# Kernel tuning notes

Measured on AMD Instinct MI355X. Metric: run time of the kernel, lower is better.

## Reference

```python
import jax, jax.numpy as jnp
import numpy as np

B, T, H, W, C = 2, 8, 20, 36, 512
NH = 4
HD = C // NH
WS = (5, 9)
EXP = (2, 4)              # window_size // 2
KP = (5, 9)               # focal unfold kernel for level k=0
PADP = (2, 4)
T2T_K, T2T_S, T2T_P = (7, 7), (3, 3), (3, 3)
FFN_HD = 1960
NWH, NWW = H // WS[0], W // WS[1]   # 4, 4
WAREA = WS[0] * WS[1]               # 45


def _valid_ind_rolled():
    wh, ww = WS
    eh, ew = EXP
    m = np.ones((4, wh, ww), np.float32)
    m[0, :wh - eh, :ww - ew] = 0   # tl
    m[1, :wh - eh, ew:] = 0        # tr
    m[2, eh:, :ww - ew] = 0        # bl
    m[3, eh:, ew:] = 0             # br
    return jnp.asarray(np.nonzero(m.reshape(-1))[0])

VALID_ROLLED = _valid_ind_rolled()  # (120,)


def unfold(x, k, s, p):
    # x: (N, Cc, Hh, Ww) -> (N, Cc*kh*kw, L); matches torch.nn.Unfold layout (c slowest).
    N, Cc, Hh, Ww = x.shape
    kh, kw = k; sh, sw = s; ph, pw = p
    xp = jnp.pad(x, ((0, 0), (0, 0), (ph, ph), (pw, pw)))
    oh = (Hh + 2 * ph - kh) // sh + 1
    ow = (Ww + 2 * pw - kw) // sw + 1
    cols = [xp[:, :, i:i + oh * sh:sh, j:j + ow * sw:sw]
            for i in range(kh) for j in range(kw)]
    patches = jnp.stack(cols, axis=2)            # (N, Cc, kh*kw, oh, ow)
    return patches.reshape(N, Cc * kh * kw, oh * ow)


def fold(patches, out_hw, k, s, p):
    # inverse of unfold (overlap-add), matches torch F.fold.
    N = patches.shape[0]
    kh, kw = k; sh, sw = s; ph, pw = p
    Hh, Ww = out_hw
    oh = (Hh + 2 * ph - kh) // sh + 1
    ow = (Ww + 2 * pw - kw) // sw + 1
    Cc = patches.shape[1] // (kh * kw)
    pr = patches.reshape(N, Cc, kh, kw, oh, ow)
    out = jnp.zeros((N, Cc, Hh + 2 * ph, Ww + 2 * pw), patches.dtype)
    for i in range(kh):
        for j in range(kw):
            out = out.at[:, :, i:i + oh * sh:sh, j:j + ow * sw:sw].add(pr[:, :, i, j])
    return out[:, :, ph:ph + Hh, pw:pw + Ww]


def layer_norm(x, g, b):
    mu = jnp.mean(x, -1, keepdims=True)
    var = jnp.var(x, -1, keepdims=True)
    return (x - mu) * jax.lax.rsqrt(var + 1e-5) * g + b


def win_part(x):
    # (B,T,H,W,C) -> (B*nW, T*wh*ww, C)
    b = x.shape[0]
    x = x.reshape(b, T, NWH, WS[0], NWW, WS[1], C)
    return x.transpose(0, 2, 4, 1, 3, 5, 6).reshape(-1, T * WAREA, C)


def to_heads(w):
    return w.reshape(-1, T, WAREA, NH, HD).transpose(0, 3, 1, 2, 4).reshape(-1, NH, T * WAREA, HD)


def block_forward(x, g1, be1, wqkv, bqkv, wproj, bproj, wpool, bpool, g2, be2, w1, bf1, w2, bf2, out_h, out_w):
    shortcut = x
    xn = layer_norm(x, g1, be1)

    # ---- coarser (pooled) focal level, k=0 (focal_level=2) ----
    wnr = xn.reshape(B, T, NWH, WS[0], NWW, WS[1], C).transpose(0, 2, 4, 1, 3, 5, 6)
    wnr = wnr.reshape(B, NWH, NWW, T, WAREA, C)
    pooled = jnp.einsum('bhwtnc,n->bhwtc', wnr, wpool) + bpool   # (B,NWH,NWW,T,C)

    # ---- window attention ----
    qkv = xn @ wqkv + bqkv                                       # (B,T,H,W,3C)
    q, k, v = jnp.split(qkv, 3, axis=-1)
    qw = to_heads(win_part(q)) * (HD ** -0.5)
    kw_, vw = to_heads(win_part(k)), to_heads(win_part(v))

    def rolled(t):
        parts = []
        for sh, sw in ((-EXP[0], -EXP[1]), (-EXP[0], EXP[1]), (EXP[0], -EXP[1]), (EXP[0], EXP[1])):
            r = jnp.roll(t, (sh, sw), axis=(2, 3))
            parts.append(win_part(r).reshape(-1, T, WAREA, NH, HD))
        cat = jnp.concatenate(parts, axis=2)                     # (B*nW, T, 4*warea, NH, HD)
        cat = jnp.take(cat.transpose(0, 3, 1, 2, 4), VALID_ROLLED, axis=3)
        return cat.reshape(-1, NH, T * VALID_ROLLED.shape[0], HD)

    k_rolled = jnp.concatenate([kw_, rolled(k)], axis=2)         # (B*nW, NH, T*165, HD)
    v_rolled = jnp.concatenate([vw, rolled(v)], axis=2)

    # pooled keys/values via focal unfold
    xp = pooled.transpose(0, 3, 1, 2, 4)                          # (B,T,NWH,NWW,C)
    qkv_p = xp @ wqkv + bqkv
    kp, vp = qkv_p[..., C:2 * C], qkv_p[..., 2 * C:]

    def unfold_kv(t):
        t = t.transpose(0, 1, 4, 2, 3).reshape(B * T, C, NWH, NWW)
        u = unfold(t, KP, (1, 1), PADP)                           # (B*T, C*45, L)
        L = u.shape[-1]
        u = u.reshape(B, T, C, KP[0], KP[1], L).transpose(0, 5, 1, 3, 4, 2)
        u = u.reshape(B * L, T, KP[0] * KP[1], NH, HD).transpose(0, 3, 1, 2, 4)
        return u.reshape(B * L, NH, T * KP[0] * KP[1], HD)

    k_all = jnp.concatenate([k_rolled, unfold_kv(kp)], axis=2)
    v_all = jnp.concatenate([v_rolled, unfold_kv(vp)], axis=2)

    attn = jnp.einsum('wnqd,wnkd->wnqk', qw, k_all)               # (B*nW, NH, T*45, N)

    # validity mask for pooled context (zero-padded unfold positions -> -100)
    ones = jnp.ones((T, 1, NWH, NWW), x.dtype)
    um = unfold(ones, KP, (1, 1), PADP)                           # (T, 45, L)
    L = um.shape[-1]
    mvals = jnp.where(um.reshape(T, KP[0] * KP[1], L).transpose(2, 0, 1).reshape(L, -1) == 0,
                      jnp.asarray(-100.0, x.dtype), jnp.asarray(0.0, x.dtype))
    n_rolled = k_rolled.shape[2]
    mask_cols = jnp.concatenate([jnp.zeros((L, n_rolled), x.dtype), mvals], axis=1)
    attn = attn + jnp.tile(mask_cols, (B, 1))[:, None, None, :]

    attn = jax.nn.softmax(attn, axis=-1)
    out = jnp.einsum('wnqk,wnkd->wnqd', attn, v_all)
    out = out.transpose(0, 2, 1, 3).reshape(-1, T * WAREA, C) @ wproj + bproj

    # window reverse + residual
    out = out.reshape(B, NWH, NWW, T, WS[0], WS[1], C)
    out = out.transpose(0, 3, 1, 4, 2, 5, 6).reshape(B, T, H, W, C)
    x = shortcut + out

    # ---- FusionFeedForward (fold/unfold re-normalized MLP) ----
    y = layer_norm(x, g2, be2).reshape(B, T * H * W, C)
    h = y @ w1 + bf1                                              # (B, n, 1960)
    nvec = ((out_h + 2 * T2T_P[0] - T2T_K[0]) // T2T_S[0] + 1) * \
           ((out_w + 2 * T2T_P[1] - T2T_K[1]) // T2T_S[1] + 1)
    bt = (B * T * H * W) // nvec
    norm_p = jnp.ones((bt, T2T_K[0] * T2T_K[1], nvec), x.dtype)
    norm_f = fold(norm_p, (out_h, out_w), T2T_K, T2T_S, T2T_P)    # (bt,1,out_h,out_w)
    h_f = fold(h.reshape(bt, nvec, FFN_HD).transpose(0, 2, 1), (out_h, out_w), T2T_K, T2T_S, T2T_P)
    h = unfold(h_f / norm_f, T2T_K, T2T_S, T2T_P).transpose(0, 2, 1).reshape(B, T * H * W, FFN_HD)
    h = jax.nn.gelu(h, approximate=False) @ w2 + bf2
    return x + h.reshape(B, T, H, W, C)


def setup_inputs() -> dict:
    key = jax.random.key(0)
    ks = jax.random.split(key, 8)
    s = 0.02
    return dict(
        x=jax.random.normal(ks[0], (B, T, H, W, C), jnp.float32),
        g1=jnp.ones((C,), jnp.float32),
        be1=jnp.zeros((C,), jnp.float32),
        wqkv=jax.random.normal(ks[1], (C, 3 * C), jnp.float32) * s,
        bqkv=jnp.zeros((3 * C,), jnp.float32),
        wproj=jax.random.normal(ks[2], (C, C), jnp.float32) * s,
        bproj=jnp.zeros((C,), jnp.float32),
        wpool=jnp.full((WAREA,), 1.0 / WAREA, jnp.float32),
        bpool=jnp.zeros((1,), jnp.float32),
        g2=jnp.ones((C,), jnp.float32),
        be2=jnp.zeros((C,), jnp.float32),
        w1=jax.random.normal(ks[3], (C, FFN_HD), jnp.float32) * s,
        bf1=jnp.zeros((FFN_HD,), jnp.float32),
        w2=jax.random.normal(ks[4], (FFN_HD, C), jnp.float32) * s,
        bf2=jnp.zeros((C,), jnp.float32),
        out_h=60,
        out_w=108,
    )


def reference(x, g1, be1, wqkv, bqkv, wproj, bproj, wpool, bpool, g2, be2, w1, bf1, w2, bf2, out_h, out_w):
    return block_forward(x, g1, be1, wqkv, bqkv, wproj, bproj, wpool, bpool,
                         g2, be2, w1, bf1, w2, bf2, out_h, out_w)
```

## Files before the change

### kernel.cpp

```cpp
#include <hip/hip_runtime.h>
#include <hip/hip_bf16.h>
#include <math.h>

typedef __hip_bfloat16 bf16;
typedef __attribute__((ext_vector_type(8))) short bf16x8;
typedef __attribute__((ext_vector_type(4))) float f32x4;

#define DEVI __device__ __forceinline__

#define C_ 512
#define NH_ 4
#define NTOK 11520
#define NKEY 1680
#define NRK 120
#define FFN_ 1960
#define ZROW (NTOK + 256)

DEVI float ldf(const bf16* p) { return __bfloat162float(*p); }
DEVI float ldf(const float* p) { return *p; }
DEVI void stw(bf16* p, float v) { *p = __float2bfloat16(v); }
DEVI void stw(float* p, float v) { *p = v; }
DEVI unsigned short f2bs(float f) { bf16 h = __float2bfloat16(f); return *(unsigned short*)&h; }

template <int DT> DEVI float ldw(const void* p, size_t i) {
  if (DT == 0) return __bfloat162float(((const bf16*)p)[i]);
  else         return ((const float*)p)[i];
}

DEVI void gload_lds16(const void* g, void* l) {
  __builtin_amdgcn_global_load_lds(
      (const __attribute__((address_space(1))) void*)g,
      (__attribute__((address_space(3))) void*)l, 16, 0, 0);
}

__global__ void k_detect(const void* __restrict__ g1, int* __restrict__ flag) {
  if (threadIdx.x == 0) {
    const unsigned short* p = (const unsigned short*)g1;
    *flag = (p[0] == 0x3F80u) ? 0 : 1;
  }
}

__global__ void k_prep(int* __restrict__ table) {
  if (threadIdx.x == 0) {
    int cnt = 0;
    for (int p = 0; p < 4; p++)
      for (int wi = 0; wi < 5; wi++)
        for (int wj = 0; wj < 9; wj++) {
          bool invalid;
          if (p == 0)      invalid = (wi < 3) && (wj < 5);
          else if (p == 1) invalid = (wi < 3) && (wj >= 4);
          else if (p == 2) invalid = (wi >= 2) && (wj < 5);
          else             invalid = (wi >= 2) && (wj >= 4);
          if (!invalid) table[cnt++] = p * 45 + wi * 9 + wj;
        }
  }
}

__global__ void k_ksrc(const int* __restrict__ vtab, int* __restrict__ ksrc) {
  int idx = blockIdx.x * 256 + threadIdx.x;
  if (idx >= 32 * NKEY) return;
  int w = idx / NKEY, j = idx % NKEY;
  int b = w >> 4, nh = (w >> 2) & 3, nw = w & 3;
  int val;
  if (j < 360) {
    int t = j / 45, pos = j % 45, wi = pos / 9, wj2 = pos % 9;
    val = ((b * 8 + t) * 20 + nh * 5 + wi) * 36 + nw * 9 + wj2;
  } else if (j < 1320) {
    int jj = j - 360;
    int t = jj / 120, r = jj % 120;
    int id = vtab[r];
    int p = id / 45, pos = id % 45, wi = pos / 9, wj2 = pos % 9;
    int sh = (p < 2) ? -2 : 2;
    int sw = (p & 1) ? 4 : -4;
    int hh = nh * 5 + wi - sh;
    if (hh < 0) hh += 20; else if (hh >= 20) hh -= 20;
    int ww2 = nw * 9 + wj2 - sw;
    if (ww2 < 0) ww2 += 36; else if (ww2 >= 36) ww2 -= 36;
    val = ((b * 8 + t) * 20 + hh) * 36 + ww2;
  } else {
    int jj = j - 1320;
    int t = jj / 45, kidx = jj % 45, ki = kidx / 9, kj = kidx % 9;
    int snh = nh + ki - 2, snw = nw + kj - 4;
    if (snh < 0 || snh >= 4 || snw < 0 || snw >= 4) val = -1;
    else val = NTOK + (b * 8 + t) * 16 + snh * 4 + snw;
  }
  ksrc[idx] = val;
}

template <int DT>
__global__ void k_wcvt(const int* __restrict__ dflag, const void* __restrict__ in,
                       bf16* __restrict__ out, int K, int N, int Npad) {
  if (*dflag != DT) return;
  __shared__ float t[64][65];
  const int n0 = blockIdx.x * 64;
  const int k0 = blockIdx.y * 64;
  const int tx = threadIdx.x & 63, tg = threadIdx.x >> 6;
#pragma unroll
  for (int r = 0; r < 16; r++) {
    int k = k0 + r * 4 + tg;
    int nn = n0 + tx;
    float v = (k < K && nn < N) ? ldw<DT>(in, (size_t)k * N + nn) : 0.f;
    t[r * 4 + tg][tx] = v;
  }
  __syncthreads();
#pragma unroll
  for (int r = 0; r < 16; r++) {
    int nn = n0 + r * 4 + tg;
    int k = k0 + tx;
    if (nn < Npad && k < K)
      out[(size_t)nn * K + k] = __float2bfloat16(t[tx][r * 4 + tg]);
  }
}

template <int DT>
__global__ void k_bcvt(const int* __restrict__ dflag, const void* __restrict__ in,
                       float* __restrict__ out, int n) {
  if (*dflag != DT) return;
  int i = blockIdx.x * 256 + threadIdx.x;
  if (i < n) out[i] = ldw<DT>(in, i);
}

__global__ void k_zrow(bf16* __restrict__ p) {
  p[blockIdx.x * 256 + threadIdx.x] = __float2bfloat16(0.f);
}

template <int DT, typename InT>
__global__ void k_ln(const int* __restrict__ dflag, const InT* __restrict__ xin,
                     const void* __restrict__ g, const void* __restrict__ be,
                     bf16* __restrict__ out) {
  if (*dflag != DT) return;
  const int tok = blockIdx.x;
  const int tid = threadIdx.x;
  const size_t base = (size_t)tok * C_;
  float v0 = ldf(xin + base + tid);
  float v1 = ldf(xin + base + tid + 256);
  float s = v0 + v1, ss = v0 * v0 + v1 * v1;
#pragma unroll
  for (int o = 32; o; o >>= 1) { s += __shfl_xor(s, o); ss += __shfl_xor(ss, o); }
  __shared__ float sh[10];
  const int lane = tid & 63, wv = tid >> 6;
  if (lane == 0) { sh[wv] = s; sh[4 + wv] = ss; }
  __syncthreads();
  if (tid == 0) {
    float a = sh[0] + sh[1] + sh[2] + sh[3];
    float q = sh[4] + sh[5] + sh[6] + sh[7];
    float mu = a * (1.0f / C_);
    float var = q * (1.0f / C_) - mu * mu;
    sh[8] = mu; sh[9] = rsqrtf(fmaxf(var, 0.f) + 1e-5f);
  }
  __syncthreads();
  float mu = sh[8], inv = sh[9];
  stw(out + base + tid,
      (v0 - mu) * inv * ldw<DT>(g, tid) + ldw<DT>(be, tid));
  stw(out + base + tid + 256,
      (v1 - mu) * inv * ldw<DT>(g, tid + 256) + ldw<DT>(be, tid + 256));
}

template <int DT>
__global__ void k_pool(const int* __restrict__ dflag, const bf16* __restrict__ xn,
                       const void* __restrict__ wpool, const void* __restrict__ bpool,
                       float* __restrict__ pooled) {
  if (*dflag != DT) return;
  int idx = blockIdx.x * blockDim.x + threadIdx.x;
  if (idx >= 256 * C_) return;
  int c = idx & (C_ - 1);
  int fw = idx >> 9;
  int nw = fw & 3, nh = (fw >> 2) & 3;
  int bt = fw >> 4;
  float acc = ldw<DT>(bpool, 0);
  for (int wi = 0; wi < 5; wi++) {
    int hh = nh * 5 + wi;
    const bf16* base = xn + (((size_t)(bt * 20 + hh)) * 36 + nw * 9) * C_ + c;
    for (int wj = 0; wj < 9; wj++)
      acc += __bfloat162float(base[(size_t)wj * C_]) * ldw<DT>(wpool, wi * 9 + wj);
  }
  pooled[idx] = acc;
}

template <int DT>
__global__ void k_gemm_small(const int* __restrict__ dflag, const float* __restrict__ A,
                             const void* __restrict__ Bw, const void* __restrict__ bias,
                             bf16* __restrict__ Cc) {
  if (*dflag != DT) return;
  __shared__ float As[8][512];
  const int n = blockIdx.x * 256 + threadIdx.x;
  const int m0 = blockIdx.y * 8;
  for (int i = threadIdx.x; i < 8 * 512; i += 256)
    As[i >> 9][i & 511] = A[(size_t)(m0 + (i >> 9)) * 512 + (i & 511)];
  __syncthreads();
  float acc[8];
  float bv = ldw<DT>(bias, n);
#pragma unroll
  for (int mm = 0; mm < 8; mm++) acc[mm] = bv;
  for (int k = 0; k < 512; k++) {
    float b = ldw<DT>(Bw, (size_t)k * 1536 + n);
#pragma unroll
    for (int mm = 0; mm < 8; mm++) acc[mm] += As[mm][k] * b;
  }
#pragma unroll
  for (int mm = 0; mm < 8; mm++)
    Cc[(size_t)(m0 + mm) * 1536 + n] = __float2bfloat16(acc[mm]);
}

template <int DT, int RES, typename OutT>
__global__ __launch_bounds__(256) void k_gemm_m(const int* __restrict__ dflag,
                                                const bf16* __restrict__ A,
                                                const bf16* __restrict__ Bt,
                                                const float* __restrict__ bias,
                                                const void* __restrict__ resid,
                                                OutT* __restrict__ out,
                                                int M, int N, int K) {
  if (dflag && *dflag != DT) return;
  __shared__ __align__(16) unsigned short As[128 * 32];
  __shared__ __align__(16) unsigned short Bs[128 * 32];
  const int tid = threadIdx.x;
  const int lane = tid & 63, wid = tid >> 6;
  const int r15 = lane & 15, quad = lane >> 4;
  const int wm = wid >> 1, wn = wid & 1;
  const int m0 = blockIdx.y * 128, n0 = blockIdx.x * 128;

  f32x4 acc[4][4];
#pragma unroll
  for (int i = 0; i < 4; i++)
#pragma unroll
    for (int j = 0; j < 4; j++)
#pragma unroll
      for (int e = 0; e < 4; e++) acc[i][j][e] = 0.f;

  const int lrow = lane >> 2, lcol = (lane & 3) * 8;

  for (int k0 = 0; k0 < K; k0 += 32) {
    int rem = K - k0;
    if (rem >= 32) {
      const bf16* ga = A + (size_t)(m0 + wid * 32 + lrow) * K + k0 + lcol;
      gload_lds16(ga, &As[wid * 1024]);
      gload_lds16(ga + (size_t)16 * K, &As[wid * 1024 + 512]);
      const bf16* gb = Bt + (size_t)(n0 + wid * 32 + lrow) * K + k0 + lcol;
      gload_lds16(gb, &Bs[wid * 1024]);
      gload_lds16(gb + (size_t)16 * K, &Bs[wid * 1024 + 512]);
    } else {
      int r = tid >> 2, c = (tid & 3) * 8;
      uint4 z = make_uint4(0, 0, 0, 0);
      uint4 a0 = z, a1 = z, b0 = z, b1 = z;
      if (c < rem) {
        a0 = *(const uint4*)(A + (size_t)(m0 + r) * K + k0 + c);
        a1 = *(const uint4*)(A + (size_t)(m0 + r + 64) * K + k0 + c);
        b0 = *(const uint4*)(Bt + (size_t)(n0 + r) * K + k0 + c);
        b1 = *(const uint4*)(Bt + (size_t)(n0 + r + 64) * K + k0 + c);
      }
      *(uint4*)&As[r * 32 + c] = a0;
      *(uint4*)&As[(r + 64) * 32 + c] = a1;
      *(uint4*)&Bs[r * 32 + c] = b0;
      *(uint4*)&Bs[(r + 64) * 32 + c] = b1;
    }
    __syncthreads();

    bf16x8 af[4], bfr[4];
#pragma unroll
    for (int mf = 0; mf < 4; mf++)
      af[mf] = *(const bf16x8*)&As[(wm * 64 + mf * 16 + r15) * 32 + quad * 8];
#pragma unroll
    for (int nf = 0; nf < 4; nf++)
      bfr[nf] = *(const bf16x8*)&Bs[(wn * 64 + nf * 16 + r15) * 32 + quad * 8];
#pragma unroll
    for (int mf = 0; mf < 4; mf++)
#pragma unroll
      for (int nf = 0; nf < 4; nf++)
        acc[mf][nf] = __builtin_amdgcn_mfma_f32_16x16x32_bf16(af[mf], bfr[nf],
                                                              acc[mf][nf], 0, 0, 0);
    __syncthreads();
  }

#pragma unroll
  for (int nf = 0; nf < 4; nf++) {
    int n = n0 + wn * 64 + nf * 16 + r15;
    if (n >= N) continue;
    float bv = bias[n];
#pragma unroll
    for (int mf = 0; mf < 4; mf++) {
      int mb = m0 + wm * 64 + mf * 16 + quad * 4;
#pragma unroll
      for (int e = 0; e < 4; e++) {
        size_t off = (size_t)(mb + e) * N + n;
        float v = acc[mf][nf][e] + bv;
        if (RES == 1) v += ldw<DT>(resid, off);
        else if (RES == 2) v += ((const float*)resid)[off];
        stw(out + off, v);
      }
    }
  }
}

#define KT 64
#define KPAD 136
#define VPAD 72
__global__ __launch_bounds__(768) void k_attn_m(const bf16* __restrict__ qkv,
                                                const int* __restrict__ ksrc,
                                                bf16* __restrict__ ao) {
  __shared__ int ks_l[NKEY];
  __shared__ __align__(16) unsigned short ktl[2][KT * KPAD];
  __shared__ __align__(16) unsigned short vtl[2][128 * VPAD];
  __shared__ __align__(16) unsigned short ptl[12 * 16 * VPAD];
  __shared__ float maskv[2][KT];

  const int tid = threadIdx.x;
  const int lane = tid & 63, wid = tid >> 6;
  const int r15 = lane & 15, quad = lane >> 4;
  const int w = blockIdx.x, qt = blockIdx.y, n = blockIdx.z;
  const int b = w >> 4, nh = (w >> 2) & 3, nw = w & 3;
  const unsigned short* qkvs = (const unsigned short*)qkv;

  for (int j = tid; j < NKEY; j += 768) ks_l[j] = ksrc[w * NKEY + j];

  bf16x8 qf[4];
  {
    int qw = qt * 192 + wid * 16 + r15;
    int qc2 = qw < 360 ? qw : 359;
    int t = qc2 / 45, pos = qc2 % 45, wi = pos / 9, wj = pos % 9;
    int tok = ((b * 8 + t) * 20 + nh * 5 + wi) * 36 + nw * 9 + wj;
    const unsigned short* qp = qkvs + (size_t)tok * 1536 + n * 128 + quad * 8;
#pragma unroll
    for (int c = 0; c < 4; c++)
      qf[c] = *(const bf16x8*)(qp + c * 32);
  }

  f32x4 of[8];
#pragma unroll
  for (int nt = 0; nt < 8; nt++)
#pragma unroll
    for (int e = 0; e < 4; e++) of[nt][e] = 0.f;
  float m_[4], l_[4];
#pragma unroll
  for (int e = 0; e < 4; e++) { m_[e] = -1e30f; l_[e] = 0.f; }

  unsigned short* ptw = &ptl[wid * 16 * VPAD];

  const bool isK = (wid < 4);
  const int kr = tid >> 2, kp = tid & 3;
  const int vr = lane, vp8 = wid - 4;
  uint4 k0, k1, k2, k3, v0, v1;
  float mreg = -30000.f;
  const unsigned short* kbase = qkvs + 512 + n * 128 + kp * 32;
  const unsigned short* vbase = qkvs + 1024 + n * 128 + vp8 * 16;

  auto load_tile = [&](int j0) {
    int cnt = NKEY - j0; if (cnt > KT) cnt = KT;
    if (isK) {
      int s0 = (kr < cnt) ? ks_l[j0 + kr] : -1;
      mreg = (s0 < 0) ? -30000.f : 0.f;
      int row = (s0 < 0) ? ZROW : s0;
      const uint4* kq = (const uint4*)(kbase + (size_t)row * 1536);
      k0 = kq[0]; k1 = kq[1]; k2 = kq[2]; k3 = kq[3];
    } else {
      int s1 = (vr < cnt) ? ks_l[j0 + vr] : -1;
      int row = (s1 < 0) ? ZROW : s1;
      const uint4* vq = (const uint4*)(vbase + (size_t)row * 1536);
      v0 = vq[0]; v1 = vq[1];
    }
  };

  auto store_tile = [&](int buf) {
    if (isK) {
      if (kp == 0) maskv[buf][kr] = mreg;
      unsigned short* kb = &ktl[buf][kr * KPAD + kp * 32];
      *(uint4*)&kb[0]  = k0;
      *(uint4*)&kb[8]  = k1;
      *(uint4*)&kb[16] = k2;
      *(uint4*)&kb[24] = k3;
    } else {
      unsigned short* vb = &vtl[buf][0];
      int d0 = vp8 * 16;
      vb[(d0 + 0) * VPAD + vr]  = (unsigned short)(v0.x & 0xFFFFu);
      vb[(d0 + 1) * VPAD + vr]  = (unsigned short)(v0.x >> 16);
      vb[(d0 + 2) * VPAD + vr]  = (unsigned short)(v0.y & 0xFFFFu);
      vb[(d0 + 3) * VPAD + vr]  = (unsigned short)(v0.y >> 16);
      vb[(d0 + 4) * VPAD + vr]  = (unsigned short)(v0.z & 0xFFFFu);
      vb[(d0 + 5) * VPAD + vr]  = (unsigned short)(v0.z >> 16);
      vb[(d0 + 6) * VPAD + vr]  = (unsigned short)(v0.w & 0xFFFFu);
      vb[(d0 + 7) * VPAD + vr]  = (unsigned short)(v0.w >> 16);
      vb[(d0 + 8) * VPAD + vr]  = (unsigned short)(v1.x & 0xFFFFu);
      vb[(d0 + 9) * VPAD + vr]  = (unsigned short)(v1.x >> 16);
      vb[(d0 + 10) * VPAD + vr] = (unsigned short)(v1.y & 0xFFFFu);
      vb[(d0 + 11) * VPAD + vr] = (unsigned short)(v1.y >> 16);
      vb[(d0 + 12) * VPAD + vr] = (unsigned short)(v1.z & 0xFFFFu);
      vb[(d0 + 13) * VPAD + vr] = (unsigned short)(v1.z >> 16);
      vb[(d0 + 14) * VPAD + vr] = (unsigned short)(v1.w & 0xFFFFu);
      vb[(d0 + 15) * VPAD + vr] = (unsigned short)(v1.w >> 16);
    }
  };

  __syncthreads();
  load_tile(0);
  store_tile(0);
  load_tile(KT);
  __syncthreads();

  int cur = 0, j0 = 0;
  while (true) {
    int nxt = j0 + KT;
    if (nxt < NKEY) {
      store_tile(cur ^ 1);
      if (nxt + KT < NKEY) load_tile(nxt + KT);
    }

    const unsigned short* ktc = &ktl[cur][0];
    const unsigned short* vtc = &vtl[cur][0];
    const float* mkc = maskv[cur];

    f32x4 sf[4];
#pragma unroll
    for (int ft = 0; ft < 4; ft++)
#pragma unroll
      for (int e = 0; e < 4; e++) sf[ft][e] = 0.f;
#pragma unroll
    for (int kc = 0; kc < 4; kc++) {
      bf16x8 a = qf[kc];
#pragma unroll
      for (int ft = 0; ft < 4; ft++) {
        bf16x8 bb = *(const bf16x8*)&ktc[(ft * 16 + r15) * KPAD + kc * 32 + quad * 8];
        sf[ft] = __builtin_amdgcn_mfma_f32_16x16x32_bf16(a, bb, sf[ft], 0, 0, 0);
      }
    }
    const float scl = 0.088388347648318447f;
#pragma unroll
    for (int ft = 0; ft < 4; ft++) {
      float mk = mkc[ft * 16 + r15];
#pragma unroll
      for (int e = 0; e < 4; e++) sf[ft][e] = sf[ft][e] * scl + mk;
    }
    float tm[4];
#pragma unroll
    for (int e = 0; e < 4; e++) {
      float v = fmaxf(fmaxf(sf[0][e], sf[1][e]), fmaxf(sf[2][e], sf[3][e]));
#pragma unroll
      for (int o = 1; o < 16; o <<= 1) v = fmaxf(v, __shfl_xor(v, o));
      tm[e] = v;
    }
#pragma unroll
    for (int e = 0; e < 4; e++) {
      float mn = fmaxf(m_[e], tm[e]);
      float alpha = __expf(m_[e] - mn);
      m_[e] = mn;
      float rs = 0.f;
#pragma unroll
      for (int ft = 0; ft < 4; ft++) {
        float pv = __expf(sf[ft][e] - mn);
        rs += pv;
        ptw[(quad * 4 + e) * VPAD + ft * 16 + r15] = f2bs(pv);
      }
      l_[e] = l_[e] * alpha + rs;
#pragma unroll
      for (int nt = 0; nt < 8; nt++) of[nt][e] *= alpha;
    }
#pragma unroll
    for (int kc = 0; kc < 2; kc++) {
      bf16x8 pa = *(const bf16x8*)&ptw[r15 * VPAD + kc * 32 + quad * 8];
#pragma unroll
      for (int nt = 0; nt < 8; nt++) {
        bf16x8 vb = *(const bf16x8*)&vtc[(nt * 16 + r15) * VPAD + kc * 32 + quad * 8];
        of[nt] = __builtin_amdgcn_mfma_f32_16x16x32_bf16(pa, vb, of[nt], 0, 0, 0);
      }
    }

    if (nxt >= NKEY) break;
    __syncthreads();
    cur ^= 1; j0 = nxt;
  }

#pragma unroll
  for (int e = 0; e < 4; e++) {
#pragma unroll
    for (int o = 1; o < 16; o <<= 1) l_[e] += __shfl_xor(l_[e], o);
  }
#pragma unroll
  for (int e = 0; e < 4; e++) {
    int qw = qt * 192 + wid * 16 + quad * 4 + e;
    if (qw >= 360) continue;
    float inv = 1.0f / l_[e];
    int t = qw / 45, pos = qw % 45, wi = pos / 9, wj = pos % 9;
    int tok = ((b * 8 + t) * 20 + nh * 5 + wi) * 36 + nw * 9 + wj;
    bf16* op = ao + (size_t)tok * 512 + n * 128 + r15;
#pragma unroll
    for (int nt = 0; nt < 8; nt++)
      stw(op + nt * 16, of[nt][e] * inv);
  }
}

__global__ void k_fold(const bf16* __restrict__ h1, float* __restrict__ hf) {
  int idx = blockIdx.x * 256 + threadIdx.x;
  if (idx >= 16 * 40 * 60 * 108) return;
  int x = idx % 108;
  int tmp = idx / 108;
  int y = tmp % 60; tmp /= 60;
  int c = tmp % 40;
  int bt = tmp / 40;
  float sum = 0.f;
  int cnt = 0;
  for (int ki = y % 3; ki < 7; ki += 3) {
    int num = y + 3 - ki;
    if (num < 0) continue;
    int oh = num / 3;
    if (oh >= 20) continue;
    for (int kj = x % 3; kj < 7; kj += 3) {
      int num2 = x + 3 - kj;
      if (num2 < 0) continue;
      int ow = num2 / 3;
      if (ow >= 36) continue;
      sum += __bfloat162float(
          h1[(size_t)(bt * 720 + oh * 36 + ow) * FFN_ + c * 49 + ki * 7 + kj]);
      cnt++;
    }
  }
  hf[idx] = sum / (float)cnt;
}

__global__ void k_unfold_gelu(const float* __restrict__ hf, bf16* __restrict__ h2) {
  int idx = blockIdx.x * 256 + threadIdx.x;
  if (idx >= NTOK * FFN_) return;
  int f = idx % FFN_;
  int token = idx / FFN_;
  int c = f / 49, k = f % 49, ki = k / 7, kj = k % 7;
  int bt = token / 720, vec = token % 720;
  int oh = vec / 36, ow = vec % 36;
  int y = oh * 3 + ki - 3, x = ow * 3 + kj - 3;
  float v = 0.f;
  if (y >= 0 && y < 60 && x >= 0 && x < 108)
    v = hf[((size_t)(bt * 40 + c) * 60 + y) * 108 + x];
  float g = 0.5f * v * (1.0f + erff(v * 0.70710678118654752f));
  stw(h2 + idx, g);
}

extern "C" void kernel_launch(void* const* d_in, const int* in_sizes, int n_in,
                              void* d_out, int out_size, void* d_ws, size_t ws_size,
                              hipStream_t stream) {
  (void)in_sizes; (void)n_in; (void)out_size; (void)ws_size;
  const void* x     = d_in[0];
  const void* g1    = d_in[1];
  const void* be1   = d_in[2];
  const void* wqkv  = d_in[3];
  const void* bqkv  = d_in[4];
  const void* wproj = d_in[5];
  const void* bproj = d_in[6];
  const void* wpool = d_in[7];
  const void* bpool = d_in[8];
  const void* g2    = d_in[9];
  const void* be2   = d_in[10];
  const void* w1    = d_in[11];
  const void* bf1   = d_in[12];
  const void* w2    = d_in[13];
  const void* bf2   = d_in[14];

  char* ws = (char*)d_ws;
  size_t off = 0;
  auto alloc = [&](size_t bytes) -> void* {
    void* p = ws + off;
    off += (bytes + 255) & ~(size_t)255;
    return p;
  };

  int*   dflag  = (int*)  alloc(256);
  int*   vtab   = (int*)  alloc(NRK * sizeof(int));
  int*   ksrc   = (int*)  alloc((size_t)32 * NKEY * sizeof(int));
  bf16*  buf2   = (bf16*) alloc((size_t)NTOK * FFN_ * 2);
  float* pooled = (float*)alloc((size_t)256 * C_ * 4);
  float* x2     = (float*)alloc((size_t)NTOK * C_ * 4);
  float* hf     = (float*)alloc((size_t)16 * 40 * 60 * 108 * 4);
  bf16*  wqkv_t = (bf16*) alloc((size_t)1536 * 512 * 2);
  bf16*  wproj_t= (bf16*) alloc((size_t)512 * 512 * 2);
  bf16*  w1_t   = (bf16*) alloc((size_t)2048 * 512 * 2);
  bf16*  w2_t   = (bf16*) alloc((size_t)512 * FFN_ * 2);
  float* bqkv_f = (float*)alloc(1536 * 4);
  float* bproj_f= (float*)alloc(512 * 4);
  float* bf1_f  = (float*)alloc(FFN_ * 4);
  float* bf2_f  = (float*)alloc(512 * 4);

  bf16* buf1 = (bf16*)d_out;
  bf16* xn = buf1;
  bf16* ao = buf1;
  bf16* y  = buf1;
  bf16* qkv = buf2;
  bf16* h1  = buf2;
  bf16* qkvpb = buf2 + (size_t)NTOK * 1536;

  k_detect<<<1, 64, 0, stream>>>(g1, dflag);
  k_prep<<<1, 64, 0, stream>>>(vtab);
  k_ksrc<<<(32 * NKEY) / 256, 256, 0, stream>>>(vtab, ksrc);
  k_zrow<<<6, 256, 0, stream>>>(qkvpb + (size_t)256 * 1536);

  k_wcvt<0><<<dim3(24, 8), 256, 0, stream>>>(dflag, wqkv, wqkv_t, 512, 1536, 1536);
  k_wcvt<1><<<dim3(24, 8), 256, 0, stream>>>(dflag, wqkv, wqkv_t, 512, 1536, 1536);
  k_wcvt<0><<<dim3(8, 8), 256, 0, stream>>>(dflag, wproj, wproj_t, 512, 512, 512);
  k_wcvt<1><<<dim3(8, 8), 256, 0, stream>>>(dflag, wproj, wproj_t, 512, 512, 512);
  k_wcvt<0><<<dim3(32, 8), 256, 0, stream>>>(dflag, w1, w1_t, 512, FFN_, 2048);
  k_wcvt<1><<<dim3(32, 8), 256, 0, stream>>>(dflag, w1, w1_t, 512, FFN_, 2048);
  k_wcvt<0><<<dim3(8, 31), 256, 0, stream>>>(dflag, w2, w2_t, FFN_, 512, 512);
  k_wcvt<1><<<dim3(8, 31), 256, 0, stream>>>(dflag, w2, w2_t, FFN_, 512, 512);
  k_bcvt<0><<<6, 256, 0, stream>>>(dflag, bqkv, bqkv_f, 1536);
  k_bcvt<1><<<6, 256, 0, stream>>>(dflag, bqkv, bqkv_f, 1536);
  k_bcvt<0><<<2, 256, 0, stream>>>(dflag, bproj, bproj_f, 512);
  k_bcvt<1><<<2, 256, 0, stream>>>(dflag, bproj, bproj_f, 512);
  k_bcvt<0><<<8, 256, 0, stream>>>(dflag, bf1, bf1_f, FFN_);
  k_bcvt<1><<<8, 256, 0, stream>>>(dflag, bf1, bf1_f, FFN_);
  k_bcvt<0><<<2, 256, 0, stream>>>(dflag, bf2, bf2_f, 512);
  k_bcvt<1><<<2, 256, 0, stream>>>(dflag, bf2, bf2_f, 512);

  k_ln<0, bf16><<<NTOK, 256, 0, stream>>>(dflag, (const bf16*)x, g1, be1, xn);
  k_ln<1, float><<<NTOK, 256, 0, stream>>>(dflag, (const float*)x, g1, be1, xn);

  k_pool<0><<<512, 256, 0, stream>>>(dflag, xn, wpool, bpool, pooled);
  k_pool<1><<<512, 256, 0, stream>>>(dflag, xn, wpool, bpool, pooled);

  k_gemm_m<0, 0, bf16><<<dim3(12, 90), 256, 0, stream>>>(
      nullptr, xn, wqkv_t, bqkv_f, nullptr, qkv, NTOK, 1536, 512);

  k_gemm_small<0><<<dim3(6, 32), 256, 0, stream>>>(dflag, pooled, wqkv, bqkv, qkvpb);
  k_gemm_small<1><<<dim3(6, 32), 256, 0, stream>>>(dflag, pooled, wqkv, bqkv, qkvpb);

  k_attn_m<<<dim3(32, 2, NH_), 768, 0, stream>>>(qkv, ksrc, ao);

  k_gemm_m<0, 1, float><<<dim3(4, 90), 256, 0, stream>>>(
      dflag, ao, wproj_t, bproj_f, x, x2, NTOK, 512, 512);
  k_gemm_m<1, 1, float><<<dim3(4, 90), 256, 0, stream>>>(
      dflag, ao, wproj_t, bproj_f, x, x2, NTOK, 512, 512);

  k_ln<0, float><<<NTOK, 256, 0, stream>>>(dflag, x2, g2, be2, y);
  k_ln<1, float><<<NTOK, 256, 0, stream>>>(dflag, x2, g2, be2, y);

  k_gemm_m<0, 0, bf16><<<dim3(16, 90), 256, 0, stream>>>(
      nullptr, y, w1_t, bf1_f, nullptr, h1, NTOK, FFN_, 512);

  k_fold<<<(16 * 40 * 60 * 108) / 256, 256, 0, stream>>>(h1, hf);

  k_unfold_gelu<<<(NTOK * FFN_) / 256, 256, 0, stream>>>(hf, h1);

  k_gemm_m<0, 2, bf16><<<dim3(4, 90), 256, 0, stream>>>(
      dflag, h1, w2_t, bf2_f, x2, (bf16*)d_out, NTOK, 512, FFN_);
  k_gemm_m<1, 2, float><<<dim3(4, 90), 256, 0, stream>>>(
      dflag, h1, w2_t, bf2_f, x2, (float*)d_out, NTOK, 512, FFN_);
}
```

Before: 587.2 us.

## Process two query sub-tiles per wave in attention to reuse K/V fragments

The attention kernel drops from 12 waves to 6 waves per block. Each wave now handles 32 query rows as two 16-row subtiles, so every K and V fragment read from LDS feeds two MFMAs. This halves the LDS reads per useful MFMA and halves the number of loader threads, with each loader fetching twice as much data. The cost is much higher register pressure (two sets of accumulators and softmax state) and fewer waves to hide latency. The grid is only 256 blocks, so per-CU occupancy also drops.

```diff
diff --git a/kernel.cpp b/kernel.cpp
--- a/kernel.cpp
+++ b/kernel.cpp
@@ -294,13 +294,22 @@
 #define KT 64
 #define KPAD 136
 #define VPAD 72
-__global__ __launch_bounds__(768) void k_attn_m(const bf16* __restrict__ qkv,
+#define VST8(VV, DD)                                              \
+  vb[(DD + 0) * VPAD + vr] = (unsigned short)(VV.x & 0xFFFFu);    \
+  vb[(DD + 1) * VPAD + vr] = (unsigned short)(VV.x >> 16);        \
+  vb[(DD + 2) * VPAD + vr] = (unsigned short)(VV.y & 0xFFFFu);    \
+  vb[(DD + 3) * VPAD + vr] = (unsigned short)(VV.y >> 16);        \
+  vb[(DD + 4) * VPAD + vr] = (unsigned short)(VV.z & 0xFFFFu);    \
+  vb[(DD + 5) * VPAD + vr] = (unsigned short)(VV.z >> 16);        \
+  vb[(DD + 6) * VPAD + vr] = (unsigned short)(VV.w & 0xFFFFu);    \
+  vb[(DD + 7) * VPAD + vr] = (unsigned short)(VV.w >> 16);
+__global__ __launch_bounds__(384) void k_attn_m(const bf16* __restrict__ qkv,
                                                 const int* __restrict__ ksrc,
                                                 bf16* __restrict__ ao) {
   __shared__ int ks_l[NKEY];
   __shared__ __align__(16) unsigned short ktl[2][KT * KPAD];
   __shared__ __align__(16) unsigned short vtl[2][128 * VPAD];
-  __shared__ __align__(16) unsigned short ptl[12 * 16 * VPAD];
+  __shared__ __align__(16) unsigned short ptl[6 * 32 * VPAD];
   __shared__ float maskv[2][KT];
 
   const int tid = threadIdx.x;
@@ -310,38 +319,43 @@
   const int b = w >> 4, nh = (w >> 2) & 3, nw = w & 3;
   const unsigned short* qkvs = (const unsigned short*)qkv;
 
-  for (int j = tid; j < NKEY; j += 768) ks_l[j] = ksrc[w * NKEY + j];
-
-  bf16x8 qf[4];
-  {
-    int qw = qt * 192 + wid * 16 + r15;
+  for (int j = tid; j < NKEY; j += 384) ks_l[j] = ksrc[w * NKEY + j];
+
+  bf16x8 qf[2][4];
+#pragma unroll
+  for (int s = 0; s < 2; s++) {
+    int qw = qt * 192 + wid * 32 + s * 16 + r15;
     int qc2 = qw < 360 ? qw : 359;
     int t = qc2 / 45, pos = qc2 % 45, wi = pos / 9, wj = pos % 9;
     int tok = ((b * 8 + t) * 20 + nh * 5 + wi) * 36 + nw * 9 + wj;
     const unsigned short* qp = qkvs + (size_t)tok * 1536 + n * 128 + quad * 8;
 #pragma unroll
     for (int c = 0; c < 4; c++)
-      qf[c] = *(const bf16x8*)(qp + c * 32);
-  }
-
-  f32x4 of[8];
-#pragma unroll
-  for (int nt = 0; nt < 8; nt++)
-#pragma unroll
-    for (int e = 0; e < 4; e++) of[nt][e] = 0.f;
-  float m_[4], l_[4];
-#pragma unroll
-  for (int e = 0; e < 4; e++) { m_[e] = -1e30f; l_[e] = 0.f; }
-
-  unsigned short* ptw = &ptl[wid * 16 * VPAD];
-
-  const bool isK = (wid < 4);
-  const int kr = tid >> 2, kp = tid & 3;
-  const int vr = lane, vp8 = wid - 4;
-  uint4 k0, k1, k2, k3, v0, v1;
+      qf[s][c] = *(const bf16x8*)(qp + c * 32);
+  }
+
+  f32x4 of[2][8];
+#pragma unroll
+  for (int s = 0; s < 2; s++)
+#pragma unroll
+    for (int nt = 0; nt < 8; nt++)
+#pragma unroll
+      for (int e = 0; e < 4; e++) of[s][nt][e] = 0.f;
+  float m_[2][4], l_[2][4];
+#pragma unroll
+  for (int s = 0; s < 2; s++)
+#pragma unroll
+    for (int e = 0; e < 4; e++) { m_[s][e] = -1e30f; l_[s][e] = 0.f; }
+
+  unsigned short* ptw = &ptl[wid * 32 * VPAD];
+
+  const bool isK = (wid < 2);
+  const int kr = tid >> 1, kp = tid & 1;
+  const int vr = lane, vp4 = wid - 2;
+  uint4 k0, k1, k2, k3, k4, k5, k6, k7, v0, v1, v2, v3;
   float mreg = -30000.f;
-  const unsigned short* kbase = qkvs + 512 + n * 128 + kp * 32;
-  const unsigned short* vbase = qkvs + 1024 + n * 128 + vp8 * 16;
+  const unsigned short* kbase = qkvs + 512 + n * 128 + kp * 64;
+  const unsigned short* vbase = qkvs + 1024 + n * 128 + vp4 * 32;
 
   auto load_tile = [&](int j0) {
     int cnt = NKEY - j0; if (cnt > KT) cnt = KT;
@@ -351,41 +365,34 @@
       int row = (s0 < 0) ? ZROW : s0;
       const uint4* kq = (const uint4*)(kbase + (size_t)row * 1536);
       k0 = kq[0]; k1 = kq[1]; k2 = kq[2]; k3 = kq[3];
+      k4 = kq[4]; k5 = kq[5]; k6 = kq[6]; k7 = kq[7];
     } else {
       int s1 = (vr < cnt) ? ks_l[j0 + vr] : -1;
       int row = (s1 < 0) ? ZROW : s1;
       const uint4* vq = (const uint4*)(vbase + (size_t)row * 1536);
-      v0 = vq[0]; v1 = vq[1];
+      v0 = vq[0]; v1 = vq[1]; v2 = vq[2]; v3 = vq[3];
     }
   };
 
   auto store_tile = [&](int buf) {
     if (isK) {
       if (kp == 0) maskv[buf][kr] = mreg;
-      unsigned short* kb = &ktl[buf][kr * KPAD + kp * 32];
+      unsigned short* kb = &ktl[buf][kr * KPAD + kp * 64];
       *(uint4*)&kb[0]  = k0;
       *(uint4*)&kb[8]  = k1;
       *(uint4*)&kb[16] = k2;
       *(uint4*)&kb[24] = k3;
+      *(uint4*)&kb[32] = k4;
+      *(uint4*)&kb[40] = k5;
+      *(uint4*)&kb[48] = k6;
+      *(uint4*)&kb[56] = k7;
     } else {
       unsigned short* vb = &vtl[buf][0];
-      int d0 = vp8 * 16;
-      vb[(d0 + 0) * VPAD + vr]  = (unsigned short)(v0.x & 0xFFFFu);
-      vb[(d0 + 1) * VPAD + vr]  = (unsigned short)(v0.x >> 16);
-      vb[(d0 + 2) * VPAD + vr]  = (unsigned short)(v0.y & 0xFFFFu);
-      vb[(d0 + 3) * VPAD + vr]  = (unsigned short)(v0.y >> 16);
-      vb[(d0 + 4) * VPAD + vr]  = (unsigned short)(v0.z & 0xFFFFu);
-      vb[(d0 + 5) * VPAD + vr]  = (unsigned short)(v0.z >> 16);
-      vb[(d0 + 6) * VPAD + vr]  = (unsigned short)(v0.w & 0xFFFFu);
-      vb[(d0 + 7) * VPAD + vr]  = (unsigned short)(v0.w >> 16);
-      vb[(d0 + 8) * VPAD + vr]  = (unsigned short)(v1.x & 0xFFFFu);
-      vb[(d0 + 9) * VPAD + vr]  = (unsigned short)(v1.x >> 16);
-      vb[(d0 + 10) * VPAD + vr] = (unsigned short)(v1.y & 0xFFFFu);
-      vb[(d0 + 11) * VPAD + vr] = (unsigned short)(v1.y >> 16);
-      vb[(d0 + 12) * VPAD + vr] = (unsigned short)(v1.z & 0xFFFFu);
-      vb[(d0 + 13) * VPAD + vr] = (unsigned short)(v1.z >> 16);
-      vb[(d0 + 14) * VPAD + vr] = (unsigned short)(v1.w & 0xFFFFu);
-      vb[(d0 + 15) * VPAD + vr] = (unsigned short)(v1.w >> 16);
+      const int d0 = vp4 * 32;
+      VST8(v0, d0)
+      VST8(v1, d0 + 8)
+      VST8(v2, d0 + 16)
+      VST8(v3, d0 + 24)
     }
   };
 
@@ -407,58 +414,65 @@
     const unsigned short* vtc = &vtl[cur][0];
     const float* mkc = maskv[cur];
 
-    f32x4 sf[4];
-#pragma unroll
-    for (int ft = 0; ft < 4; ft++)
-#pragma unroll
-      for (int e = 0; e < 4; e++) sf[ft][e] = 0.f;
+    f32x4 sf[2][4];
+#pragma unroll
+    for (int s = 0; s < 2; s++)
+#pragma unroll
+      for (int ft = 0; ft < 4; ft++)
+#pragma unroll
+        for (int e = 0; e < 4; e++) sf[s][ft][e] = 0.f;
 #pragma unroll
     for (int kc = 0; kc < 4; kc++) {
-      bf16x8 a = qf[kc];
 #pragma unroll
       for (int ft = 0; ft < 4; ft++) {
         bf16x8 bb = *(const bf16x8*)&ktc[(ft * 16 + r15) * KPAD + kc * 32 + quad * 8];
-        sf[ft] = __builtin_amdgcn_mfma_f32_16x16x32_bf16(a, bb, sf[ft], 0, 0, 0);
+        sf[0][ft] = __builtin_amdgcn_mfma_f32_16x16x32_bf16(qf[0][kc], bb, sf[0][ft], 0, 0, 0);
+        sf[1][ft] = __builtin_amdgcn_mfma_f32_16x16x32_bf16(qf[1][kc], bb, sf[1][ft], 0, 0, 0);
       }
     }
     const float scl = 0.088388347648318447f;
 #pragma unroll
-    for (int ft = 0; ft < 4; ft++) {
-      float mk = mkc[ft * 16 + r15];
-#pragma unroll
-      for (int e = 0; e < 4; e++) sf[ft][e] = sf[ft][e] * scl + mk;
-    }
-    float tm[4];
-#pragma unroll
-    for (int e = 0; e < 4; e++) {
-      float v = fmaxf(fmaxf(sf[0][e], sf[1][e]), fmaxf(sf[2][e], sf[3][e]));
-#pragma unroll
-      for (int o = 1; o < 16; o <<= 1) v = fmaxf(v, __shfl_xor(v, o));
-      tm[e] = v;
-    }
-#pragma unroll
-    for (int e = 0; e < 4; e++) {
-      float mn = fmaxf(m_[e], tm[e]);
-      float alpha = __expf(m_[e] - mn);
-      m_[e] = mn;
-      float rs = 0.f;
+    for (int s = 0; s < 2; s++) {
 #pragma unroll
       for (int ft = 0; ft < 4; ft++) {
-        float pv = __expf(sf[ft][e] - mn);
-        rs += pv;
-        ptw[(quad * 4 + e) * VPAD + ft * 16 + r15] = f2bs(pv);
+        float mk = mkc[ft * 16 + r15];
+#pragma unroll
+        for (int e = 0; e < 4; e++) sf[s][ft][e] = sf[s][ft][e] * scl + mk;
       }
-      l_[e] = l_[e] * alpha + rs;
-#pragma unroll
-      for (int nt = 0; nt < 8; nt++) of[nt][e] *= alpha;
+      float tm[4];
+#pragma unroll
+      for (int e = 0; e < 4; e++) {
+        float v = fmaxf(fmaxf(sf[s][0][e], sf[s][1][e]), fmaxf(sf[s][2][e], sf[s][3][e]));
+#pragma unroll
+        for (int o = 1; o < 16; o <<= 1) v = fmaxf(v, __shfl_xor(v, o));
+        tm[e] = v;
+      }
+#pragma unroll
+      for (int e = 0; e < 4; e++) {
+        float mn = fmaxf(m_[s][e], tm[e]);
+        float alpha = __expf(m_[s][e] - mn);
+        m_[s][e] = mn;
+        float rs = 0.f;
+#pragma unroll
+        for (int ft = 0; ft < 4; ft++) {
+          float pv = __expf(sf[s][ft][e] - mn);
+          rs += pv;
+          ptw[(s * 16 + quad * 4 + e) * VPAD + ft * 16 + r15] = f2bs(pv);
+        }
+        l_[s][e] = l_[s][e] * alpha + rs;
+#pragma unroll
+        for (int nt = 0; nt < 8; nt++) of[s][nt][e] *= alpha;
+      }
     }
 #pragma unroll
     for (int kc = 0; kc < 2; kc++) {
-      bf16x8 pa = *(const bf16x8*)&ptw[r15 * VPAD + kc * 32 + quad * 8];
+      bf16x8 pa0 = *(const bf16x8*)&ptw[r15 * VPAD + kc * 32 + quad * 8];
+      bf16x8 pa1 = *(const bf16x8*)&ptw[(16 + r15) * VPAD + kc * 32 + quad * 8];
 #pragma unroll
       for (int nt = 0; nt < 8; nt++) {
-        bf16x8 vb = *(const bf16x8*)&vtc[(nt * 16 + r15) * VPAD + kc * 32 + quad * 8];
-        of[nt] = __builtin_amdgcn_mfma_f32_16x16x32_bf16(pa, vb, of[nt], 0, 0, 0);
+        bf16x8 vv = *(const bf16x8*)&vtc[(nt * 16 + r15) * VPAD + kc * 32 + quad * 8];
+        of[0][nt] = __builtin_amdgcn_mfma_f32_16x16x32_bf16(pa0, vv, of[0][nt], 0, 0, 0);
+        of[1][nt] = __builtin_amdgcn_mfma_f32_16x16x32_bf16(pa1, vv, of[1][nt], 0, 0, 0);
       }
     }
 
@@ -468,22 +482,26 @@
   }
 
 #pragma unroll
-  for (int e = 0; e < 4; e++) {
-#pragma unroll
-    for (int o = 1; o < 16; o <<= 1) l_[e] += __shfl_xor(l_[e], o);
-  }
-#pragma unroll
-  for (int e = 0; e < 4; e++) {
-    int qw = qt * 192 + wid * 16 + quad * 4 + e;
-    if (qw >= 360) continue;
-    float inv = 1.0f / l_[e];
-    int t = qw / 45, pos = qw % 45, wi = pos / 9, wj = pos % 9;
-    int tok = ((b * 8 + t) * 20 + nh * 5 + wi) * 36 + nw * 9 + wj;
-    bf16* op = ao + (size_t)tok * 512 + n * 128 + r15;
-#pragma unroll
-    for (int nt = 0; nt < 8; nt++)
-      stw(op + nt * 16, of[nt][e] * inv);
-  }
+  for (int s = 0; s < 2; s++)
+#pragma unroll
+    for (int e = 0; e < 4; e++) {
+#pragma unroll
+      for (int o = 1; o < 16; o <<= 1) l_[s][e] += __shfl_xor(l_[s][e], o);
+    }
+#pragma unroll
+  for (int s = 0; s < 2; s++)
+#pragma unroll
+    for (int e = 0; e < 4; e++) {
+      int qw = qt * 192 + wid * 32 + s * 16 + quad * 4 + e;
+      if (qw >= 360) continue;
+      float inv = 1.0f / l_[s][e];
+      int t = qw / 45, pos = qw % 45, wi = pos / 9, wj = pos % 9;
+      int tok = ((b * 8 + t) * 20 + nh * 5 + wi) * 36 + nw * 9 + wj;
+      bf16* op = ao + (size_t)tok * 512 + n * 128 + r15;
+#pragma unroll
+      for (int nt = 0; nt < 8; nt++)
+        stw(op + nt * 16, of[s][nt][e] * inv);
+    }
 }
 
 __global__ void k_fold(const bf16* __restrict__ h1, float* __restrict__ hf) {
@@ -616,7 +634,7 @@
   k_gemm_small<0><<<dim3(6, 32), 256, 0, stream>>>(dflag, pooled, wqkv, bqkv, qkvpb);
   k_gemm_small<1><<<dim3(6, 32), 256, 0, stream>>>(dflag, pooled, wqkv, bqkv, qkvpb);
 
-  k_attn_m<<<dim3(32, 2, NH_), 768, 0, stream>>>(qkv, ksrc, ao);
+  k_attn_m<<<dim3(32, 2, NH_), 384, 0, stream>>>(qkv, ksrc, ao);
 
   k_gemm_m<0, 1, float><<<dim3(4, 90), 256, 0, stream>>>(
       dflag, ao, wproj_t, bproj_f, x, x2, NTOK, 512, 512);
```

After: 613.2 us. 4.4% more time.
